# Optimization experiments

Hardware: AMD Instinct MI355X
Metric: run time of the kernel (lower is better)

Reference implementation:

```python
import jax, jax.numpy as jnp
import numpy as np

B, T, C, H = 4, 4096, 768, 64  # batch, seq, embed_size, head_size


def setup_inputs() -> dict:
    key = jax.random.key(0)
    kx, kq, kk, kv = jax.random.split(key, 4)
    s = 1.0 / np.sqrt(C)
    return {
        "x": jax.random.normal(kx, (B, T, C), dtype=jnp.float32),
        "Wq": jax.random.normal(kq, (C, H), dtype=jnp.float32) * s,
        "Wk": jax.random.normal(kk, (C, H), dtype=jnp.float32) * s,
        "Wv": jax.random.normal(kv, (C, H), dtype=jnp.float32) * s,
    }


def reference(x, Wq, Wk, Wv):
    Bx, Tx, Cx = x.shape
    Q = x @ Wq  # [B, T, H]
    K = x @ Wk
    V = x @ Wv
    # NOTE: original scales by sqrt(C) = sqrt(embed_size), not head_size
    scores = jnp.einsum('bqh,bkh->bqk', Q, K) / jnp.sqrt(jnp.asarray(Cx, x.dtype))
    causal = jnp.tril(jnp.ones((Tx, Tx), dtype=bool))
    scores = jnp.where(causal, scores, -jnp.inf)
    weights = jax.nn.softmax(scores, axis=-1)
    # dropout = identity in eval mode
    return jnp.einsum('bqk,bkh->bqh', weights, V)
```

## Files before the change

kernel.cpp:

```cpp
#include <hip/hip_runtime.h>

typedef __bf16 bf16x8 __attribute__((ext_vector_type(8)));
typedef float f32x4 __attribute__((ext_vector_type(4)));
typedef unsigned int u32x4 __attribute__((ext_vector_type(4)));

#define MFMA16(a,b,c) __builtin_amdgcn_mfma_f32_16x16x32_bf16(a,b,c,0,0,0)

__device__ __forceinline__ unsigned short f2b(float x){
  __bf16 b = (__bf16)x;
  return __builtin_bit_cast(unsigned short, b);
}
__device__ __forceinline__ float b2f(unsigned short u){
  return __builtin_bit_cast(float, ((unsigned)u)<<16);
}
__device__ __forceinline__ unsigned cvtpk(float lo, float hi){
  unsigned r;
  asm("v_cvt_pk_bf16_f32 %0, %1, %2" : "=v"(r) : "v"(lo), "v"(hi));
  return r;
}

__device__ __forceinline__ void gld16(const void* g, void* l){
  __builtin_amdgcn_global_load_lds(
      (const __attribute__((address_space(1))) unsigned int*)g,
      (__attribute__((address_space(3))) unsigned int*)l, 16, 0, 0);
}

__global__ __launch_bounds__(256) void pack_w(const float* __restrict__ Wq,
                                              const float* __restrict__ Wk,
                                              const float* __restrict__ Wv,
                                              unsigned short* __restrict__ Wt){
  int idx = blockIdx.x*256 + threadIdx.x;
  int n = idx/768, c = idx - n*768;
  const float* W = (n < 64) ? Wq : ((n < 128) ? Wk : Wv);
  Wt[n*768 + c] = f2b(W[c*64 + (n & 63)]);
}

__global__ __launch_bounds__(256,2) void qkv_proj(const float* __restrict__ x,
                                                  const unsigned short* __restrict__ Wt,
                                                  unsigned short* __restrict__ Qb,
                                                  unsigned short* __restrict__ Kb,
                                                  unsigned short* __restrict__ Vt){
  __shared__ __attribute__((aligned(16))) float Xl[2][32*64];
  __shared__ __attribute__((aligned(16))) unsigned short Wl[2][192*64];
  const int tid = threadIdx.x;
  const int w = tid>>6, l = tid&63, quad = l>>4, lr = l&15;
  const int row0 = blockIdx.x*32;

  auto stage = [&](int kk, int buf){
#pragma unroll
    for(int i=0;i<2;i++){
      int n = (w*2+i)*4 + (l>>4);
      int sc = (l&15) ^ (n&15);
      gld16(x + (size_t)(row0+n)*768 + kk*64 + sc*4, &Xl[buf][(w*2+i)*256]);
    }
#pragma unroll
    for(int i=0;i<6;i++){
      int gr0 = (w*6+i)*8;
      int n = gr0 + (l>>3);
      int sc = (l&7) ^ (l>>3);
      gld16(Wt + (size_t)n*768 + kk*64 + sc*8, &Wl[buf][gr0*64]);
    }
  };

  f32x4 acc[2][3];
#pragma unroll
  for(int mt=0;mt<2;mt++)
#pragma unroll
    for(int nt=0;nt<3;nt++) acc[mt][nt] = (f32x4)0.0f;

  stage(0, 0);
  int buf = 0;
  for(int kk=0; kk<12; kk++){
    __syncthreads();
    if(kk+1 < 12) stage(kk+1, buf^1);
    bf16x8 a[2][2];
#pragma unroll
    for(int mt=0;mt<2;mt++){
#pragma unroll
      for(int ks=0;ks<2;ks++){
        int c = ks*8 + quad*2;
        f32x4 v0 = *(const f32x4*)&Xl[buf][(mt*16+lr)*64 + ((c   ^ lr)&15)*4];
        f32x4 v1 = *(const f32x4*)&Xl[buf][(mt*16+lr)*64 + (((c+1)^ lr)&15)*4];
#pragma unroll
        for(int jj=0;jj<4;jj++){ a[mt][ks][jj] = (__bf16)v0[jj]; a[mt][ks][4+jj] = (__bf16)v1[jj]; }
      }
    }
#pragma unroll
    for(int nt=0;nt<3;nt++){
#pragma unroll
      for(int ks=0;ks<2;ks++){
        int n = w*48 + nt*16 + lr;
        int q = ks*4 + quad;
        bf16x8 bfr = *(const bf16x8*)&Wl[buf][n*64 + ((q ^ (lr&7))&7)*8];
#pragma unroll
        for(int mt=0;mt<2;mt++) acc[mt][nt] = MFMA16(a[mt][ks], bfr, acc[mt][nt]);
      }
    }
    buf ^= 1;
  }
  const int b_ = row0>>12;
  const float sc = (float)(1.4426950408889634 * 0.03608439182435161);
#pragma unroll
  for(int mt=0;mt<2;mt++){
    const int t0 = (row0 & 4095) + mt*16 + quad*4;
#pragma unroll
    for(int nt=0;nt<3;nt++){
      int g = w*48 + nt*16 + lr;
      if(g < 64){
#pragma unroll
        for(int r=0;r<4;r++) Qb[((size_t)(b_*4096 + t0 + r))*64 + g] = f2b(acc[mt][nt][r]*sc);
      } else if(g < 128){
#pragma unroll
        for(int r=0;r<4;r++) Kb[((size_t)(b_*4096 + t0 + r))*64 + (g-64)] = f2b(acc[mt][nt][r]);
      } else {
        ushort4 pk;
        pk.x = f2b(acc[mt][nt][0]); pk.y = f2b(acc[mt][nt][1]);
        pk.z = f2b(acc[mt][nt][2]); pk.w = f2b(acc[mt][nt][3]);
        *(ushort4*)&Vt[((size_t)(b_*64 + (g-128)))*4096 + t0] = pk;
      }
    }
  }
}

__device__ __forceinline__ void attn_stage(const unsigned short* kbp, const unsigned short* vbp,
                                           int kt, int w, int r8, int cj,
                                           unsigned short* Kl, unsigned short* Vl){
#pragma unroll
  for(int i=0;i<2;i++){
    int row = w*16 + i*8 + r8;
    int gc = cj ^ r8;
    gld16(kbp + ((size_t)(kt*64 + row))*64 + gc*8, Kl + (w*16 + i*8)*64);
    gld16(vbp + ((size_t)row)*4096 + kt*64 + gc*8, Vl + (w*16 + i*8)*64);
  }
}

__global__ __launch_bounds__(256,3) void attn(const unsigned short* __restrict__ Qb,
                                              const unsigned short* __restrict__ Kb,
                                              const unsigned short* __restrict__ Vt,
                                              unsigned short* __restrict__ Opart,
                                              float* __restrict__ Rpart){
  __shared__ __attribute__((aligned(16))) unsigned short Kl[2][64*64];
  __shared__ __attribute__((aligned(16))) unsigned short Vl[2][64*64];
  const int tid = threadIdx.x;
  const int w = tid>>6, l = tid&63, quad = l>>4, lr = l&15;
  const int xx = 143 - blockIdx.x;
  int i = 0, accu = 0;
  while(true){ int c = (i+4)>>2; if(accu + c > xx) break; accu += c; i++; }
  const int r = xx - accu;
  const int b = blockIdx.y;
  const int q0 = i*128;
  const int lo = r*8;
  const int hi = min(lo+8, 2*i+2);
  const int diag0 = 2*i;
  const int r8 = l>>3, cj = l&7;
  const int lx = lr & 7;
  bf16x8 aq[2][2];
#pragma unroll
  for(int m=0;m<2;m++){
    const unsigned short* qp = Qb + ((size_t)(b*4096 + q0 + w*32 + m*16 + lr))*64 + quad*8;
    aq[m][0] = *(const bf16x8*)qp;
    aq[m][1] = *(const bf16x8*)(qp + 32);
  }
  u32x4 ow;
  {
    unsigned oc = (lr == 0) ? 0x3F803F80u : 0u;
    ow[0]=oc; ow[1]=oc; ow[2]=oc; ow[3]=oc;
  }
  const bf16x8 ones = __builtin_bit_cast(bf16x8, ow);

  f32x4 o_[2][4];
  f32x4 o_ext[2];
#pragma unroll
  for(int m=0;m<2;m++){
    o_ext[m] = (f32x4)0.0f;
#pragma unroll
    for(int nt=0;nt<4;nt++) o_[m][nt] = (f32x4)0.0f;
  }
  const unsigned short* kbp = Kb + ((size_t)b*4096)*64;
  const unsigned short* vbp = Vt + ((size_t)b*64)*4096;

  attn_stage(kbp, vbp, lo, w, r8, cj, Kl[0], Vl[0]);
  int cur = 0;
  const int qg0 = q0 + w*32;
  for(int kt = lo; kt < hi; kt++){
    __syncthreads();
    if(kt+1 < hi) attn_stage(kbp, vbp, kt+1, w, r8, cj, Kl[cur^1], Vl[cur^1]);
    const bool diag = (kt >= diag0);
    bf16x8 ap[2][2];
#pragma unroll
    for(int ks=0;ks<2;ks++){
      f32x4 sv[2][2];
#pragma unroll
      for(int cc=0;cc<2;cc++){
        int ct = ks*2 + cc;
        int base = (ct*16+lr)*64;
        bf16x8 k0 = *(const bf16x8*)&Kl[cur][base + ((quad    ^ lx)<<3)];
        bf16x8 k1 = *(const bf16x8*)&Kl[cur][base + (((4+quad)^ lx)<<3)];
#pragma unroll
        for(int m=0;m<2;m++){
          f32x4 z = (f32x4)0.0f;
          z = MFMA16(k0, aq[m][0], z);
          sv[m][cc] = MFMA16(k1, aq[m][1], z);
        }
      }
#pragma unroll
      for(int m=0;m<2;m++){
        int qg = qg0 + m*16 + lr;
        float e[2][4];
#pragma unroll
        for(int cc=0;cc<2;cc++){
          int kb = kt*64 + (ks*2+cc)*16 + quad*4;
#pragma unroll
          for(int rr=0;rr<4;rr++){
            float p = __builtin_exp2f(sv[m][cc][rr]);
            e[cc][rr] = (!diag || (kb + rr <= qg)) ? p : 0.0f;
          }
        }
        unsigned a0 = cvtpk(e[0][0], e[0][1]);
        unsigned a1 = cvtpk(e[0][2], e[0][3]);
        unsigned b0 = cvtpk(e[1][0], e[1][1]);
        unsigned b1 = cvtpk(e[1][2], e[1][3]);
        asm("v_permlane32_swap_b32 %0, %1" : "+v"(a0), "+v"(b0));
        asm("v_permlane16_swap_b32 %0, %1" : "+v"(a0), "+v"(b0));
        asm("v_permlane32_swap_b32 %0, %1" : "+v"(a1), "+v"(b1));
        asm("v_permlane16_swap_b32 %0, %1" : "+v"(a1), "+v"(b1));
        u32x4 wv; wv[0] = a0; wv[1] = a1; wv[2] = b0; wv[3] = b1;
        ap[m][ks] = __builtin_bit_cast(bf16x8, wv);
      }
    }
#pragma unroll
    for(int ks=0;ks<2;ks++){
#pragma unroll
      for(int nt=0;nt<4;nt++){
        bf16x8 bv = *(const bf16x8*)&Vl[cur][(nt*16+lr)*64 + (((ks*4+quad)^lx)<<3)];
#pragma unroll
        for(int m=0;m<2;m++) o_[m][nt] = MFMA16(ap[m][ks], bv, o_[m][nt]);
      }
#pragma unroll
      for(int m=0;m<2;m++) o_ext[m] = MFMA16(ap[m][ks], ones, o_ext[m]);
    }
    cur ^= 1;
  }
  const int slab = r*4 + b;
#pragma unroll
  for(int m=0;m<2;m++){
    if(lr == 0){
#pragma unroll
      for(int rr=0;rr<4;rr++)
        Rpart[slab*4096 + q0 + w*32 + m*16 + quad*4 + rr] = o_ext[m][rr];
    }
#pragma unroll
    for(int rr=0;rr<4;rr++){
      int row = q0 + w*32 + m*16 + quad*4 + rr;
#pragma unroll
      for(int nt=0;nt<4;nt++)
        Opart[((size_t)(slab*4096 + row))*64 + nt*16 + lr] = f2b(o_[m][nt][rr]);
    }
  }
}

__global__ __launch_bounds__(256) void combine(const unsigned short* __restrict__ Opart,
                                               const float* __restrict__ Rpart,
                                               float* __restrict__ out){
  int gid = blockIdx.x*256 + threadIdx.x;
  int cg = gid & 15;
  int t  = (gid >> 4) & 4095;
  int b  = gid >> 16;
  int i  = t >> 7;
  int np = (i + 4) >> 2;
  float o0=0.f, o1=0.f, o2=0.f, o3=0.f, rsum=0.f;
  for(int r=0; r<np; r++){
    int slab = r*4 + b;
    rsum += Rpart[slab*4096 + t];
    ushort4 u = *(const ushort4*)(Opart + ((size_t)(slab*4096 + t))*64 + cg*4);
    o0 += b2f(u.x); o1 += b2f(u.y); o2 += b2f(u.z); o3 += b2f(u.w);
  }
  float inv = 1.0f/rsum;
  f32x4 v; v[0]=o0*inv; v[1]=o1*inv; v[2]=o2*inv; v[3]=o3*inv;
  *(f32x4*)(out + ((size_t)(b*4096 + t))*64 + cg*4) = v;
}

extern "C" void kernel_launch(void* const* d_in, const int* in_sizes, int n_in,
                              void* d_out, int out_size, void* d_ws, size_t ws_size,
                              hipStream_t stream){
  const float* x  = (const float*)d_in[0];
  const float* Wq = (const float*)d_in[1];
  const float* Wk = (const float*)d_in[2];
  const float* Wv = (const float*)d_in[3];
  float* out = (float*)d_out;
  char* ws = (char*)d_ws;
  unsigned short* Wt = (unsigned short*)(ws);
  unsigned short* Qb = (unsigned short*)(ws + 0x080000);
  unsigned short* Kb = (unsigned short*)(ws + 0x280000);
  unsigned short* Vt = (unsigned short*)(ws + 0x480000);
  unsigned short* Opart = (unsigned short*)(ws + 0x680000);
  float* Rpart = (float*)(ws + 0x1680000);
  hipLaunchKernelGGL(pack_w,   dim3(576),     dim3(256), 0, stream, Wq, Wk, Wv, Wt);
  hipLaunchKernelGGL(qkv_proj, dim3(512),     dim3(256), 0, stream, x, Wt, Qb, Kb, Vt);
  hipLaunchKernelGGL(attn,     dim3(144, 4),  dim3(256), 0, stream, Qb, Kb, Vt, Opart, Rpart);
  hipLaunchKernelGGL(combine,  dim3(1024),    dim3(256), 0, stream, Opart, Rpart, out);
}
```

Before: 132.1 us.

## Fuse split-K combine into attention via atomic last-block reduction

Removes the separate combine kernel. Each attention block now increments a per-(query tile, batch) counter after writing its partial output, and the last block to arrive reduces the partials and writes the normalized result. The grid is flattened to 1D with batch interleaved, so the heavy causal tiles are scheduled first across all batches. This saves one kernel launch and the tail of a separate pass, in exchange for atomics, fences, and serialized reduction work on the final block of each tile.

Result: slower. 223.8 us (+69.5%).

```diff
diff --git a/kernel.cpp b/kernel.cpp
--- a/kernel.cpp
+++ b/kernel.cpp
@@ -28,8 +28,10 @@
 __global__ __launch_bounds__(256) void pack_w(const float* __restrict__ Wq,
                                               const float* __restrict__ Wk,
                                               const float* __restrict__ Wv,
-                                              unsigned short* __restrict__ Wt){
+                                              unsigned short* __restrict__ Wt,
+                                              int* __restrict__ cnt){
   int idx = blockIdx.x*256 + threadIdx.x;
+  if(idx < 128) cnt[idx] = 0;
   int n = idx/768, c = idx - n*768;
   const float* W = (n < 64) ? Wq : ((n < 128) ? Wk : Wv);
   Wt[n*768 + c] = f2b(W[c*64 + (n & 63)]);
@@ -138,16 +140,20 @@
                                               const unsigned short* __restrict__ Kb,
                                               const unsigned short* __restrict__ Vt,
                                               unsigned short* __restrict__ Opart,
-                                              float* __restrict__ Rpart){
+                                              float* __restrict__ Rpart,
+                                              float* __restrict__ outp,
+                                              int* __restrict__ cnt){
   __shared__ __attribute__((aligned(16))) unsigned short Kl[2][64*64];
   __shared__ __attribute__((aligned(16))) unsigned short Vl[2][64*64];
   const int tid = threadIdx.x;
   const int w = tid>>6, l = tid&63, quad = l>>4, lr = l&15;
-  const int xx = 143 - blockIdx.x;
+  const int n_ = blockIdx.x;
+  const int b = (n_ & 7) >> 1;
+  const int slot = (n_ >> 3)*2 + (n_ & 1);
+  const int xx = 143 - slot;
   int i = 0, accu = 0;
   while(true){ int c = (i+4)>>2; if(accu + c > xx) break; accu += c; i++; }
   const int r = xx - accu;
-  const int b = blockIdx.y;
   const int q0 = i*128;
   const int lo = r*8;
   const int hi = min(lo+8, 2*i+2);
@@ -257,27 +263,27 @@
         Opart[((size_t)(slab*4096 + row))*64 + nt*16 + lr] = f2b(o_[m][nt][rr]);
     }
   }
-}
-
-__global__ __launch_bounds__(256) void combine(const unsigned short* __restrict__ Opart,
-                                               const float* __restrict__ Rpart,
-                                               float* __restrict__ out){
-  int gid = blockIdx.x*256 + threadIdx.x;
-  int cg = gid & 15;
-  int t  = (gid >> 4) & 4095;
-  int b  = gid >> 16;
-  int i  = t >> 7;
-  int np = (i + 4) >> 2;
-  float o0=0.f, o1=0.f, o2=0.f, o3=0.f, rsum=0.f;
-  for(int r=0; r<np; r++){
-    int slab = r*4 + b;
-    rsum += Rpart[slab*4096 + t];
-    ushort4 u = *(const ushort4*)(Opart + ((size_t)(slab*4096 + t))*64 + cg*4);
-    o0 += b2f(u.x); o1 += b2f(u.y); o2 += b2f(u.z); o3 += b2f(u.w);
-  }
-  float inv = 1.0f/rsum;
-  f32x4 v; v[0]=o0*inv; v[1]=o1*inv; v[2]=o2*inv; v[3]=o3*inv;
-  *(f32x4*)(out + ((size_t)(b*4096 + t))*64 + cg*4) = v;
+  __threadfence();
+  __shared__ int tk;
+  if(tid == 0) tk = atomicAdd(&cnt[i*4 + b], 1);
+  __syncthreads();
+  const int np_ = (i + 4) >> 2;
+  if(tk != np_ - 1) return;
+  __threadfence();
+  for(int task = tid; task < 2048; task += 256){
+    int trow = q0 + (task >> 4);
+    int cg = task & 15;
+    float o0=0.f, o1=0.f, o2=0.f, o3=0.f, rsum=0.f;
+    for(int rr2=0; rr2<np_; rr2++){
+      int sl = rr2*4 + b;
+      rsum += Rpart[sl*4096 + trow];
+      ushort4 u = *(const ushort4*)(Opart + ((size_t)(sl*4096 + trow))*64 + cg*4);
+      o0 += b2f(u.x); o1 += b2f(u.y); o2 += b2f(u.z); o3 += b2f(u.w);
+    }
+    float inv = 1.0f/rsum;
+    f32x4 v; v[0]=o0*inv; v[1]=o1*inv; v[2]=o2*inv; v[3]=o3*inv;
+    *(f32x4*)(outp + ((size_t)(b*4096 + trow))*64 + cg*4) = v;
+  }
 }
 
 extern "C" void kernel_launch(void* const* d_in, const int* in_sizes, int n_in,
@@ -295,8 +301,8 @@
   unsigned short* Vt = (unsigned short*)(ws + 0x480000);
   unsigned short* Opart = (unsigned short*)(ws + 0x680000);
   float* Rpart = (float*)(ws + 0x1680000);
-  hipLaunchKernelGGL(pack_w,   dim3(576),     dim3(256), 0, stream, Wq, Wk, Wv, Wt);
-  hipLaunchKernelGGL(qkv_proj, dim3(512),     dim3(256), 0, stream, x, Wt, Qb, Kb, Vt);
-  hipLaunchKernelGGL(attn,     dim3(144, 4),  dim3(256), 0, stream, Qb, Kb, Vt, Opart, Rpart);
-  hipLaunchKernelGGL(combine,  dim3(1024),    dim3(256), 0, stream, Opart, Rpart, out);
-}
+  int* cnt = (int*)(ws + 0x1700000);
+  hipLaunchKernelGGL(pack_w,   dim3(576),  dim3(256), 0, stream, Wq, Wk, Wv, Wt, cnt);
+  hipLaunchKernelGGL(qkv_proj, dim3(512),  dim3(256), 0, stream, x, Wt, Qb, Kb, Vt);
+  hipLaunchKernelGGL(attn,     dim3(576),  dim3(256), 0, stream, Qb, Kb, Vt, Opart, Rpart, out, cnt);
+}
```

## Load projection weights from global into registers and split attention into finer KV chunks

Applied to the files above, without the earlier changes.

In the QKV projection, the weight tile no longer goes through LDS. Each wave now loads its weight fragments straight from global memory into double-buffered registers, which frees LDS and raises the occupancy hint from 2 to 3. The attention work split goes from chunks of 8 KV tiles to chunks of 5, which raises the grid from 144 to 224 blocks per batch and the occupancy hint to 4. This should balance load across CUs better. In exchange, there are more partial slabs to write and combine, more workspace is needed, and register pressure may rise.

Result: no change. 134.3 us (+1.7%).

```diff
diff --git a/kernel.cpp b/kernel.cpp
--- a/kernel.cpp
+++ b/kernel.cpp
@@ -35,32 +35,32 @@
   Wt[n*768 + c] = f2b(W[c*64 + (n & 63)]);
 }
 
-__global__ __launch_bounds__(256,2) void qkv_proj(const float* __restrict__ x,
+__global__ __launch_bounds__(256,3) void qkv_proj(const float* __restrict__ x,
                                                   const unsigned short* __restrict__ Wt,
                                                   unsigned short* __restrict__ Qb,
                                                   unsigned short* __restrict__ Kb,
                                                   unsigned short* __restrict__ Vt){
   __shared__ __attribute__((aligned(16))) float Xl[2][32*64];
-  __shared__ __attribute__((aligned(16))) unsigned short Wl[2][192*64];
   const int tid = threadIdx.x;
   const int w = tid>>6, l = tid&63, quad = l>>4, lr = l&15;
   const int row0 = blockIdx.x*32;
-
-  auto stage = [&](int kk, int buf){
+  const int wn = w*48 + lr;
+
+  auto stageX = [&](int kk, int buf){
 #pragma unroll
     for(int i=0;i<2;i++){
       int n = (w*2+i)*4 + (l>>4);
       int sc = (l&15) ^ (n&15);
       gld16(x + (size_t)(row0+n)*768 + kk*64 + sc*4, &Xl[buf][(w*2+i)*256]);
     }
-#pragma unroll
-    for(int i=0;i<6;i++){
-      int gr0 = (w*6+i)*8;
-      int n = gr0 + (l>>3);
-      int sc = (l&7) ^ (l>>3);
-      gld16(Wt + (size_t)n*768 + kk*64 + sc*8, &Wl[buf][gr0*64]);
-    }
   };
+  auto loadW = [&](int kk, bf16x8 (&wf)[3][2]){
+#pragma unroll
+    for(int nt=0;nt<3;nt++)
+#pragma unroll
+      for(int ks=0;ks<2;ks++)
+        wf[nt][ks] = *(const bf16x8*)(Wt + (size_t)(wn + nt*16)*768 + kk*64 + (ks*4+quad)*8);
+  };
 
   f32x4 acc[2][3];
 #pragma unroll
@@ -68,11 +68,13 @@
 #pragma unroll
     for(int nt=0;nt<3;nt++) acc[mt][nt] = (f32x4)0.0f;
 
-  stage(0, 0);
-  int buf = 0;
-  for(int kk=0; kk<12; kk++){
+  bf16x8 wfA[3][2], wfB[3][2];
+  loadW(0, wfA);
+  stageX(0, 0);
+
+  auto qstep = [&](int kk, int buf, bf16x8 (&wfc)[3][2], bf16x8 (&wfn)[3][2]){
     __syncthreads();
-    if(kk+1 < 12) stage(kk+1, buf^1);
+    if(kk+1 < 12){ stageX(kk+1, buf^1); loadW(kk+1, wfn); }
     bf16x8 a[2][2];
 #pragma unroll
     for(int mt=0;mt<2;mt++){
@@ -86,18 +88,18 @@
       }
     }
 #pragma unroll
-    for(int nt=0;nt<3;nt++){
-#pragma unroll
-      for(int ks=0;ks<2;ks++){
-        int n = w*48 + nt*16 + lr;
-        int q = ks*4 + quad;
-        bf16x8 bfr = *(const bf16x8*)&Wl[buf][n*64 + ((q ^ (lr&7))&7)*8];
-#pragma unroll
-        for(int mt=0;mt<2;mt++) acc[mt][nt] = MFMA16(a[mt][ks], bfr, acc[mt][nt]);
-      }
-    }
-    buf ^= 1;
-  }
+    for(int nt=0;nt<3;nt++)
+#pragma unroll
+      for(int ks=0;ks<2;ks++)
+#pragma unroll
+        for(int mt=0;mt<2;mt++) acc[mt][nt] = MFMA16(a[mt][ks], wfc[nt][ks], acc[mt][nt]);
+  };
+
+  for(int kk=0; kk<12; kk+=2){
+    qstep(kk,   0, wfA, wfB);
+    qstep(kk+1, 1, wfB, wfA);
+  }
+
   const int b_ = row0>>12;
   const float sc = (float)(1.4426950408889634 * 0.03608439182435161);
 #pragma unroll
@@ -134,7 +136,7 @@
   }
 }
 
-__global__ __launch_bounds__(256,3) void attn(const unsigned short* __restrict__ Qb,
+__global__ __launch_bounds__(256,4) void attn(const unsigned short* __restrict__ Qb,
                                               const unsigned short* __restrict__ Kb,
                                               const unsigned short* __restrict__ Vt,
                                               unsigned short* __restrict__ Opart,
@@ -143,14 +145,14 @@
   __shared__ __attribute__((aligned(16))) unsigned short Vl[2][64*64];
   const int tid = threadIdx.x;
   const int w = tid>>6, l = tid&63, quad = l>>4, lr = l&15;
-  const int xx = 143 - blockIdx.x;
+  const int xx = 223 - blockIdx.x;
   int i = 0, accu = 0;
-  while(true){ int c = (i+4)>>2; if(accu + c > xx) break; accu += c; i++; }
+  while(true){ int c = (2*i+6)/5; if(accu + c > xx) break; accu += c; i++; }
   const int r = xx - accu;
   const int b = blockIdx.y;
   const int q0 = i*128;
-  const int lo = r*8;
-  const int hi = min(lo+8, 2*i+2);
+  const int lo = r*5;
+  const int hi = min(lo+5, 2*i+2);
   const int diag0 = 2*i;
   const int r8 = l>>3, cj = l&7;
   const int lx = lr & 7;
@@ -267,7 +269,7 @@
   int t  = (gid >> 4) & 4095;
   int b  = gid >> 16;
   int i  = t >> 7;
-  int np = (i + 4) >> 2;
+  int np = (2*i + 6)/5;
   float o0=0.f, o1=0.f, o2=0.f, o3=0.f, rsum=0.f;
   for(int r=0; r<np; r++){
     int slab = r*4 + b;
@@ -294,9 +296,9 @@
   unsigned short* Kb = (unsigned short*)(ws + 0x280000);
   unsigned short* Vt = (unsigned short*)(ws + 0x480000);
   unsigned short* Opart = (unsigned short*)(ws + 0x680000);
-  float* Rpart = (float*)(ws + 0x1680000);
+  float* Rpart = (float*)(ws + 0x2280000);
   hipLaunchKernelGGL(pack_w,   dim3(576),     dim3(256), 0, stream, Wq, Wk, Wv, Wt);
   hipLaunchKernelGGL(qkv_proj, dim3(512),     dim3(256), 0, stream, x, Wt, Qb, Kb, Vt);
-  hipLaunchKernelGGL(attn,     dim3(144, 4),  dim3(256), 0, stream, Qb, Kb, Vt, Opart, Rpart);
+  hipLaunchKernelGGL(attn,     dim3(224, 4),  dim3(256), 0, stream, Qb, Kb, Vt, Opart, Rpart);
   hipLaunchKernelGGL(combine,  dim3(1024),    dim3(256), 0, stream, Opart, Rpart, out);
 }
```
